# Performance work log

Measured on AMD Instinct MI355X. Metric: run time of the kernel, lower is better.

The kernel has to match this reference:

```python
import jax, jax.numpy as jnp
import numpy as np

BETA = 1.0
EPS_MU = 1e-6
EPS_LOG = 1e-8
D_DIM = 2048
M_EVENTS = 16384
T_HORIZON = 100


def setup_inputs() -> dict:
    key = jax.random.key(0)
    k1, k2 = jax.random.split(key)
    # sorted event times in [0, T_HORIZON)
    t_events = jnp.sort(jax.random.uniform(k1, (M_EVENTS,), jnp.float32) * T_HORIZON)
    marks = jax.random.randint(k2, (M_EVENTS,), 0, D_DIM)  # int marks in {0..D-1}
    # learned params, init exactly as in torch module
    log_mu = jnp.full((D_DIM,), -3.0, jnp.float32)
    log_alpha = jnp.full((D_DIM, D_DIM), -4.0, jnp.float32)
    return {
        "t_events": t_events,
        "marks": marks,
        "T_max": T_HORIZON,
        "log_mu": log_mu,
        "log_alpha": log_alpha,
    }


def _loglik(t_events, log_mu, log_alpha, marks, T_max, beta=BETA):
    mu = jax.nn.softplus(log_mu) + EPS_MU          # [D]
    alpha = jax.nn.softplus(log_alpha)             # [D, D]
    D = mu.shape[0]
    # dt[0] = 0 so the first step leaves S (= zeros) untouched, matching the
    # torch loop which skips decay at n == 0.
    dt = jnp.concatenate([jnp.zeros((1,), t_events.dtype), jnp.diff(t_events)])  # [M]

    def step(S, xs):
        dt_n, d = xs
        S = jnp.exp(-beta * dt_n) * S              # exponential decay of state [D]
        lam_d = mu[d] + alpha[d] @ S               # intensity at event's mark
        S = S.at[d].add(1.0)                       # self-excitation bump
        return S, jnp.log(lam_d + EPS_LOG)

    _, log_lams = jax.lax.scan(step, jnp.zeros((D,), mu.dtype), (dt, marks))

    # compensator integral term
    T = jnp.asarray(T_max, t_events.dtype)
    one_minus_exp = 1.0 - jnp.exp(-beta * (T - t_events))          # [M]
    contrib = jax.ops.segment_sum(one_minus_exp, marks, num_segments=D)  # [D]
    integral = mu * T + alpha @ (contrib / beta)                   # [D]
    return log_lams.sum() - integral.sum()


def reference(t_events, marks, T_max, log_mu, log_alpha):
    return _loglik(t_events, log_mu, log_alpha, marks, T_max)
```

## Files before the change

kernel.cpp:

```cpp
#include <hip/hip_runtime.h>
#include <math.h>

#define D_DIM 2048
#define M_EV  16384
#define LCH   32
#define CCH   (M_EV / LCH)
#define SEG   32
#define NSEG  (CCH / SEG)
#define BETA  1.0f

__device__ __forceinline__ float softplus_f(float x){
  float e = __expf(-fabsf(x));
  return fmaxf(x, 0.0f) + __logf(1.0f + e);
}

__device__ __forceinline__ unsigned short f2bf(float f){
  unsigned b = __float_as_uint(f);
  return (unsigned short)((b + 0x7FFFu + ((b >> 16) & 1u)) >> 16);
}
__device__ __forceinline__ float bf2f(unsigned short u){
  return __uint_as_float(((unsigned)u) << 16);
}

__device__ __forceinline__ float decode_T(const void* p){
  unsigned bits = *(const unsigned*)p;
  float fv = __uint_as_float(bits);
  return (fv >= 1e-3f && fv <= 1e7f) ? fv : (float)(int)bits;
}

__device__ __forceinline__ float wave_red(float v){
  #pragma unroll
  for (int o = 32; o > 0; o >>= 1) v += __shfl_down(v, o);
  return v;
}

__global__ void k_small(const float* __restrict__ t, const int* __restrict__ m,
                        const void* Tp, const float* __restrict__ log_mu,
                        float* __restrict__ muw, float* __restrict__ contrib,
                        float* __restrict__ SL, float* __restrict__ dchunk,
                        float* __restrict__ cumdec, float* __restrict__ Aseg,
                        float* __restrict__ acc){
  const int b = blockIdx.x, tid = threadIdx.x;
  if (b < 8){
    int j = b*256 + tid;
    float v = softplus_f(log_mu[j]) + 1e-6f;
    muw[j] = v;
    float s = wave_red(v);
    if ((tid & 63) == 0) atomicAdd(&acc[2], s);
  } else if (b < 72){
    int i = (b-8)*256 + tid;
    int d = m[i];
    float ti = t[i];
    float T = decode_T(Tp);
    atomicAdd(&contrib[d], 1.0f - __expf(-BETA * (T - ti)));
    int c = i >> 5;
    if (c < CCH - 1){
      float tn = t[(c+1)*LCH];
      atomicAdd(&SL[(size_t)c * D_DIM + d], __expf(-BETA * (tn - ti)));
    }
  } else {
    int c = (b-72)*256 + tid;
    float tc = t[c*LCH];
    dchunk[c] = (c < CCH-1) ? __expf(-BETA * (t[(c+1)*LCH] - tc)) : 1.0f;
    int s0c = (c >> 5) << 5;
    cumdec[c] = __expf(-BETA * (tc - t[s0c*LCH]));
    if (b == 72 && tid < NSEG){
      int s = tid;
      Aseg[s] = (s < NSEG-1)
        ? __expf(-BETA * (t[(s+1)*SEG*LCH] - t[s*SEG*LCH])) : 1.0f;
    }
  }
}

__global__ void k_scan_alpha(float* __restrict__ SL,
                             const float* __restrict__ dchunk,
                             float* __restrict__ Carry,
                             const float* __restrict__ la,
                             const float* __restrict__ contrib,
                             unsigned short* __restrict__ sA,
                             float* __restrict__ acc){
  const int b = blockIdx.x, tid = threadIdx.x;
  if (b < 128){
    const int seg = b >> 3, jb = b & 7;
    const int j = jb*256 + tid;
    const int c0 = seg * SEG;
    const size_t base = (size_t)c0 * D_DIM + j;
    float u = 0.f;
    float cur[4], nxt[4];
    #pragma unroll
    for (int q = 0; q < 4; ++q) cur[q] = SL[base + (size_t)q * D_DIM];
    for (int g = 0; g < SEG; g += 4){
      #pragma unroll
      for (int q = 0; q < 4; ++q)
        nxt[q] = (g+4 < SEG) ? SL[base + (size_t)(g+4+q) * D_DIM] : 0.f;
      #pragma unroll
      for (int q = 0; q < 4; ++q){
        int c = c0 + g + q;
        float l = cur[q];
        SL[(size_t)c * D_DIM + j] = u;
        u = fmaf(dchunk[c], u, l);
      }
      #pragma unroll
      for (int q = 0; q < 4; ++q) cur[q] = nxt[q];
    }
    Carry[(size_t)seg * D_DIM + j] = u;
    return;
  }
  const int nthreads = 512*256;
  int atid = (b-128)*256 + tid;
  const float4* la4 = (const float4*)la;
  ushort4* sA4 = (ushort4*)sA;
  float p = 0.f;
  #pragma unroll
  for (int u = 0; u < 8; ++u){
    int i4 = atid + u * nthreads;
    float4 x = la4[i4];
    float4 sp;
    sp.x = softplus_f(x.x); sp.y = softplus_f(x.y);
    sp.z = softplus_f(x.z); sp.w = softplus_f(x.w);
    ushort4 h;
    h.x = f2bf(sp.x); h.y = f2bf(sp.y); h.z = f2bf(sp.z); h.w = f2bf(sp.w);
    sA4[i4] = h;
    int col = (i4 * 4) & (D_DIM - 1);
    p = fmaf(sp.x, contrib[col+0], p);
    p = fmaf(sp.y, contrib[col+1], p);
    p = fmaf(sp.z, contrib[col+2], p);
    p = fmaf(sp.w, contrib[col+3], p);
  }
  __shared__ float red[4];
  float w = wave_red(p);
  int lane = tid & 63, wid = tid >> 6;
  if (lane == 0) red[wid] = w;
  __syncthreads();
  if (tid == 0) atomicAdd(&acc[1], red[0]+red[1]+red[2]+red[3]);
}

__global__ __launch_bounds__(512) void k_events(
    const float* __restrict__ t, const int* __restrict__ m,
    const unsigned short* __restrict__ sA, const float* __restrict__ muw,
    const float* __restrict__ SL, const float* __restrict__ Carry,
    const float* __restrict__ Aseg,
    const float* __restrict__ cumdec, float* __restrict__ acc,
    const void* Tp, float* __restrict__ out){
  __shared__ float S0[D_DIM];
  __shared__ float tl[LCH];
  __shared__ int   ml[LCH];
  __shared__ float wred[8];
  const int tid = threadIdx.x;
  const int c = blockIdx.x;
  const int seg = c >> 5;
  const float cd = cumdec[c];

  {
    const float4 sv = *(const float4*)(SL + (size_t)c * D_DIM + tid*4);
    float4 e = {0.f, 0.f, 0.f, 0.f};
    float wgt = 1.f;
    for (int s = seg - 1; s >= 0; --s){
      const float4 cr = *(const float4*)(Carry + (size_t)s * D_DIM + tid*4);
      e.x = fmaf(cr.x, wgt, e.x); e.y = fmaf(cr.y, wgt, e.y);
      e.z = fmaf(cr.z, wgt, e.z); e.w = fmaf(cr.w, wgt, e.w);
      wgt *= Aseg[s];
    }
    float4 s;
    s.x = fmaf(e.x, cd, sv.x); s.y = fmaf(e.y, cd, sv.y);
    s.z = fmaf(e.z, cd, sv.z); s.w = fmaf(e.w, cd, sv.w);
    *(float4*)&S0[tid*4] = s;
  }
  if (tid < LCH){
    ml[tid] = m[c*LCH + tid];
    tl[tid] = t[c*LCH + tid];
  }
  __syncthreads();

  const int l = tid & 63, w = tid >> 6;
  const int l4 = l * 4;

  float4 s0[8];
  #pragma unroll
  for (int u = 0; u < 8; ++u) s0[u] = *(const float4*)&S0[u*256 + l4];

  const float t0 = tl[0];
  float lgw = 0.f;
  #pragma unroll
  for (int q = 0; q < 4; ++q){
    const int k = w*4 + q;
    const int d = ml[k];
    const unsigned short* row = sA + (size_t)d * D_DIM;
    float p = 0.f;
    #pragma unroll
    for (int u = 0; u < 8; ++u){
      ushort4 a = *(const ushort4*)(row + u*256 + l4);
      p = fmaf(bf2f(a.x), s0[u].x, p);
      p = fmaf(bf2f(a.y), s0[u].y, p);
      p = fmaf(bf2f(a.z), s0[u].z, p);
      p = fmaf(bf2f(a.w), s0[u].w, p);
    }
    const float tk = tl[k];
    float g = 0.f;
    if (l < k) g = bf2f(row[ml[l]]) * __expf(tl[l] - tk);
    p = fmaf(p, __expf(t0 - tk), g);
    float v = wave_red(p);
    if (l == 0) lgw += __logf(muw[d] + v + 1e-8f);
  }
  if (l == 0) wred[w] = lgw;
  __syncthreads();
  if (tid == 0){
    float lg = ((wred[0]+wred[1])+(wred[2]+wred[3]))
             + ((wred[4]+wred[5])+(wred[6]+wred[7]));
    atomicAdd(&acc[0], lg);
    __threadfence();
    unsigned old = atomicAdd((unsigned*)&acc[3], 1u);
    if (old == CCH - 1){
      float a0 = atomicAdd(&acc[0], 0.0f);
      float a1 = atomicAdd(&acc[1], 0.0f);
      float a2 = atomicAdd(&acc[2], 0.0f);
      float T = decode_T(Tp);
      out[0] = a0 - (T * a2 + a1 * (1.0f / BETA));
    }
  }
}

extern "C" void kernel_launch(void* const* d_in, const int* in_sizes, int n_in,
                              void* d_out, int out_size, void* d_ws, size_t ws_size,
                              hipStream_t stream) {
  const float* t_events  = (const float*)d_in[0];
  const int*   marks     = (const int*)  d_in[1];
  const void*  Tp        =               d_in[2];
  const float* log_mu    = (const float*)d_in[3];
  const float* log_alpha = (const float*)d_in[4];
  float* out = (float*)d_out;

  float* ws      = (float*)d_ws;
  float* SL      = ws;
  float* contrib = SL + (size_t)CCH * D_DIM;
  float* acc     = contrib + D_DIM;
  float* Carry   = acc + 16;
  float* muw     = Carry + (size_t)NSEG * D_DIM;
  float* dchunk  = muw + D_DIM;
  float* cumdec  = dchunk + CCH;
  float* Aseg    = cumdec + CCH;
  unsigned short* sA = (unsigned short*)(Aseg + NSEG);

  size_t zero_floats = (size_t)CCH * D_DIM + D_DIM + 16;
  hipMemsetAsync(d_ws, 0, zero_floats * sizeof(float), stream);

  k_small     <<<74, 256, 0, stream>>>(t_events, marks, Tp, log_mu, muw,
                                       contrib, SL, dchunk, cumdec, Aseg, acc);
  k_scan_alpha<<<640, 256, 0, stream>>>(SL, dchunk, Carry, log_alpha,
                                        contrib, sA, acc);
  k_events    <<<CCH, 512, 0, stream>>>(t_events, marks, sA, muw,
                                        SL, Carry, Aseg, cumdec, acc, Tp, out);
}
```

Baseline: 113.5 us.

## Fuse memset and three kernels into one cooperative kernel with grid syncs

Replaces the memset plus three separate launches with a single cooperative kernel of 512 blocks × 256 threads. Grid-wide syncs separate the zeroing, prep, alpha-softplus/scan and event phases, and the final combine moves behind a last grid sync instead of an atomic counter. The aim is to remove launch gaps and the memset. In exchange it pays for several grid barriers, halves threads per block in the event phase (8 events per wave), and needs all 512 blocks to be co-resident.

```diff
diff --git a/kernel.cpp b/kernel.cpp
--- a/kernel.cpp
+++ b/kernel.cpp
@@ -1,4 +1,5 @@
 #include <hip/hip_runtime.h>
+#include <hip/hip_cooperative_groups.h>
 #include <math.h>
 
 #define D_DIM 2048
@@ -9,6 +10,12 @@
 #define NSEG  (CCH / SEG)
 #define BETA  1.0f
 
+#define NBLK  CCH
+#define NTHR  256
+#define TOTTHR (NBLK * NTHR)
+
+namespace cg = cooperative_groups;
+
 __device__ __forceinline__ float softplus_f(float x){
   float e = __expf(-fabsf(x));
   return fmaxf(x, 0.0f) + __logf(1.0f + e);
@@ -34,21 +41,38 @@
   return v;
 }
 
-__global__ void k_small(const float* __restrict__ t, const int* __restrict__ m,
-                        const void* Tp, const float* __restrict__ log_mu,
-                        float* __restrict__ muw, float* __restrict__ contrib,
-                        float* __restrict__ SL, float* __restrict__ dchunk,
-                        float* __restrict__ cumdec, float* __restrict__ Aseg,
-                        float* __restrict__ acc){
-  const int b = blockIdx.x, tid = threadIdx.x;
-  if (b < 8){
-    int j = b*256 + tid;
-    float v = softplus_f(log_mu[j]) + 1e-6f;
-    muw[j] = v;
+__global__ __launch_bounds__(NTHR, 2) void k_fused(
+    const float* __restrict__ t, const int* __restrict__ m,
+    const void* Tp, const float* __restrict__ log_mu,
+    const float* __restrict__ la,
+    float* __restrict__ muw, float* __restrict__ contrib,
+    float* __restrict__ SL, float* __restrict__ dchunk,
+    float* __restrict__ cumdec, float* __restrict__ Aseg,
+    float* __restrict__ Carry, unsigned short* __restrict__ sA,
+    float* __restrict__ acc, float* __restrict__ out)
+{
+  cg::grid_group grid = cg::this_grid();
+  const int b   = blockIdx.x;
+  const int tid = threadIdx.x;
+  const int gtid = b * NTHR + tid;
+
+  {
+    const float4 z = make_float4(0.f, 0.f, 0.f, 0.f);
+    float4* SL4 = (float4*)SL;
+    SL4[gtid] = z;
+    SL4[gtid + TOTTHR] = z;
+    if (gtid < D_DIM / 4) ((float4*)contrib)[gtid] = z;
+    if (gtid < 16) acc[gtid] = 0.f;
+  }
+  grid.sync();
+
+  if (gtid < 2048){
+    float v = softplus_f(log_mu[gtid]) + 1e-6f;
+    muw[gtid] = v;
     float s = wave_red(v);
     if ((tid & 63) == 0) atomicAdd(&acc[2], s);
-  } else if (b < 72){
-    int i = (b-8)*256 + tid;
+  } else if (gtid < 2048 + M_EV){
+    int i = gtid - 2048;
     int d = m[i];
     float ti = t[i];
     float T = decode_T(Tp);
@@ -58,34 +82,53 @@
       float tn = t[(c+1)*LCH];
       atomicAdd(&SL[(size_t)c * D_DIM + d], __expf(-BETA * (tn - ti)));
     }
-  } else {
-    int c = (b-72)*256 + tid;
+  } else if (gtid < 2048 + M_EV + CCH){
+    int c = gtid - (2048 + M_EV);
     float tc = t[c*LCH];
     dchunk[c] = (c < CCH-1) ? __expf(-BETA * (t[(c+1)*LCH] - tc)) : 1.0f;
     int s0c = (c >> 5) << 5;
     cumdec[c] = __expf(-BETA * (tc - t[s0c*LCH]));
-    if (b == 72 && tid < NSEG){
-      int s = tid;
-      Aseg[s] = (s < NSEG-1)
-        ? __expf(-BETA * (t[(s+1)*SEG*LCH] - t[s*SEG*LCH])) : 1.0f;
-    }
-  }
-}
-
-__global__ void k_scan_alpha(float* __restrict__ SL,
-                             const float* __restrict__ dchunk,
-                             float* __restrict__ Carry,
-                             const float* __restrict__ la,
-                             const float* __restrict__ contrib,
-                             unsigned short* __restrict__ sA,
-                             float* __restrict__ acc){
-  const int b = blockIdx.x, tid = threadIdx.x;
-  if (b < 128){
-    const int seg = b >> 3, jb = b & 7;
-    const int j = jb*256 + tid;
-    const int c0 = seg * SEG;
+  } else if (gtid < 2048 + M_EV + CCH + NSEG){
+    int s = gtid - (2048 + M_EV + CCH);
+    Aseg[s] = (s < NSEG-1)
+      ? __expf(-BETA * (t[(s+1)*SEG*LCH] - t[s*SEG*LCH])) : 1.0f;
+  }
+  grid.sync();
+
+  {
+    const float4* la4 = (const float4*)la;
+    ushort4* sA4 = (ushort4*)sA;
+    float p = 0.f;
+    #pragma unroll
+    for (int u = 0; u < 8; ++u){
+      int i4 = gtid + u * TOTTHR;
+      float4 x = la4[i4];
+      float4 sp;
+      sp.x = softplus_f(x.x); sp.y = softplus_f(x.y);
+      sp.z = softplus_f(x.z); sp.w = softplus_f(x.w);
+      ushort4 h;
+      h.x = f2bf(sp.x); h.y = f2bf(sp.y); h.z = f2bf(sp.z); h.w = f2bf(sp.w);
+      sA4[i4] = h;
+      int col = (i4 * 4) & (D_DIM - 1);
+      p = fmaf(sp.x, contrib[col+0], p);
+      p = fmaf(sp.y, contrib[col+1], p);
+      p = fmaf(sp.z, contrib[col+2], p);
+      p = fmaf(sp.w, contrib[col+3], p);
+    }
+    __shared__ float red[4];
+    float wsum = wave_red(p);
+    int lane = tid & 63, wid = tid >> 6;
+    if (lane == 0) red[wid] = wsum;
+    __syncthreads();
+    if (tid == 0) atomicAdd(&acc[1], red[0]+red[1]+red[2]+red[3]);
+  }
+
+  if (gtid < NSEG * D_DIM){
+    const int seg = gtid >> 11;
+    const int j   = gtid & (D_DIM - 1);
+    const int c0  = seg * SEG;
     const size_t base = (size_t)c0 * D_DIM + j;
-    float u = 0.f;
+    float u2 = 0.f;
     float cur[4], nxt[4];
     #pragma unroll
     for (int q = 0; q < 4; ++q) cur[q] = SL[base + (size_t)q * D_DIM];
@@ -97,126 +140,99 @@
       for (int q = 0; q < 4; ++q){
         int c = c0 + g + q;
         float l = cur[q];
-        SL[(size_t)c * D_DIM + j] = u;
-        u = fmaf(dchunk[c], u, l);
+        SL[(size_t)c * D_DIM + j] = u2;
+        u2 = fmaf(dchunk[c], u2, l);
       }
       #pragma unroll
       for (int q = 0; q < 4; ++q) cur[q] = nxt[q];
     }
-    Carry[(size_t)seg * D_DIM + j] = u;
-    return;
-  }
-  const int nthreads = 512*256;
-  int atid = (b-128)*256 + tid;
-  const float4* la4 = (const float4*)la;
-  ushort4* sA4 = (ushort4*)sA;
-  float p = 0.f;
-  #pragma unroll
-  for (int u = 0; u < 8; ++u){
-    int i4 = atid + u * nthreads;
-    float4 x = la4[i4];
-    float4 sp;
-    sp.x = softplus_f(x.x); sp.y = softplus_f(x.y);
-    sp.z = softplus_f(x.z); sp.w = softplus_f(x.w);
-    ushort4 h;
-    h.x = f2bf(sp.x); h.y = f2bf(sp.y); h.z = f2bf(sp.z); h.w = f2bf(sp.w);
-    sA4[i4] = h;
-    int col = (i4 * 4) & (D_DIM - 1);
-    p = fmaf(sp.x, contrib[col+0], p);
-    p = fmaf(sp.y, contrib[col+1], p);
-    p = fmaf(sp.z, contrib[col+2], p);
-    p = fmaf(sp.w, contrib[col+3], p);
-  }
-  __shared__ float red[4];
-  float w = wave_red(p);
-  int lane = tid & 63, wid = tid >> 6;
-  if (lane == 0) red[wid] = w;
-  __syncthreads();
-  if (tid == 0) atomicAdd(&acc[1], red[0]+red[1]+red[2]+red[3]);
-}
-
-__global__ __launch_bounds__(512) void k_events(
-    const float* __restrict__ t, const int* __restrict__ m,
-    const unsigned short* __restrict__ sA, const float* __restrict__ muw,
-    const float* __restrict__ SL, const float* __restrict__ Carry,
-    const float* __restrict__ Aseg,
-    const float* __restrict__ cumdec, float* __restrict__ acc,
-    const void* Tp, float* __restrict__ out){
-  __shared__ float S0[D_DIM];
-  __shared__ float tl[LCH];
-  __shared__ int   ml[LCH];
-  __shared__ float wred[8];
-  const int tid = threadIdx.x;
-  const int c = blockIdx.x;
-  const int seg = c >> 5;
-  const float cd = cumdec[c];
+    Carry[(size_t)seg * D_DIM + j] = u2;
+  }
+  grid.sync();
 
   {
-    const float4 sv = *(const float4*)(SL + (size_t)c * D_DIM + tid*4);
-    float4 e = {0.f, 0.f, 0.f, 0.f};
-    float wgt = 1.f;
-    for (int s = seg - 1; s >= 0; --s){
-      const float4 cr = *(const float4*)(Carry + (size_t)s * D_DIM + tid*4);
-      e.x = fmaf(cr.x, wgt, e.x); e.y = fmaf(cr.y, wgt, e.y);
-      e.z = fmaf(cr.z, wgt, e.z); e.w = fmaf(cr.w, wgt, e.w);
-      wgt *= Aseg[s];
-    }
-    float4 s;
-    s.x = fmaf(e.x, cd, sv.x); s.y = fmaf(e.y, cd, sv.y);
-    s.z = fmaf(e.z, cd, sv.z); s.w = fmaf(e.w, cd, sv.w);
-    *(float4*)&S0[tid*4] = s;
-  }
-  if (tid < LCH){
-    ml[tid] = m[c*LCH + tid];
-    tl[tid] = t[c*LCH + tid];
-  }
-  __syncthreads();
-
-  const int l = tid & 63, w = tid >> 6;
-  const int l4 = l * 4;
-
-  float4 s0[8];
-  #pragma unroll
-  for (int u = 0; u < 8; ++u) s0[u] = *(const float4*)&S0[u*256 + l4];
-
-  const float t0 = tl[0];
-  float lgw = 0.f;
-  #pragma unroll
-  for (int q = 0; q < 4; ++q){
-    const int k = w*4 + q;
-    const int d = ml[k];
-    const unsigned short* row = sA + (size_t)d * D_DIM;
-    float p = 0.f;
-    #pragma unroll
-    for (int u = 0; u < 8; ++u){
-      ushort4 a = *(const ushort4*)(row + u*256 + l4);
-      p = fmaf(bf2f(a.x), s0[u].x, p);
-      p = fmaf(bf2f(a.y), s0[u].y, p);
-      p = fmaf(bf2f(a.z), s0[u].z, p);
-      p = fmaf(bf2f(a.w), s0[u].w, p);
-    }
-    const float tk = tl[k];
-    float g = 0.f;
-    if (l < k) g = bf2f(row[ml[l]]) * __expf(tl[l] - tk);
-    p = fmaf(p, __expf(t0 - tk), g);
-    float v = wave_red(p);
-    if (l == 0) lgw += __logf(muw[d] + v + 1e-8f);
-  }
-  if (l == 0) wred[w] = lgw;
-  __syncthreads();
-  if (tid == 0){
-    float lg = ((wred[0]+wred[1])+(wred[2]+wred[3]))
-             + ((wred[4]+wred[5])+(wred[6]+wred[7]));
-    atomicAdd(&acc[0], lg);
-    __threadfence();
-    unsigned old = atomicAdd((unsigned*)&acc[3], 1u);
-    if (old == CCH - 1){
-      float a0 = atomicAdd(&acc[0], 0.0f);
-      float a1 = atomicAdd(&acc[1], 0.0f);
-      float a2 = atomicAdd(&acc[2], 0.0f);
-      float T = decode_T(Tp);
-      out[0] = a0 - (T * a2 + a1 * (1.0f / BETA));
-    }
+    __shared__ float S0[D_DIM];
+    __shared__ float tl[LCH];
+    __shared__ int   ml[LCH];
+    __shared__ float wred[4];
+    const int c = b;
+    const int seg = c >> 5;
+    const float cd = cumdec[c];
+    {
+      const size_t rowc = (size_t)c * D_DIM;
+      const int col = tid * 4;
+      float4 sv0 = *(const float4*)(SL + rowc + col);
+      float4 sv1 = *(const float4*)(SL + rowc + 1024 + col);
+      float4 e0 = make_float4(0,0,0,0), e1 = make_float4(0,0,0,0);
+      float wgt = 1.f;
+      for (int s = seg - 1; s >= 0; --s){
+        const float4 cr0 = *(const float4*)(Carry + (size_t)s * D_DIM + col);
+        const float4 cr1 = *(const float4*)(Carry + (size_t)s * D_DIM + 1024 + col);
+        e0.x = fmaf(cr0.x, wgt, e0.x); e0.y = fmaf(cr0.y, wgt, e0.y);
+        e0.z = fmaf(cr0.z, wgt, e0.z); e0.w = fmaf(cr0.w, wgt, e0.w);
+        e1.x = fmaf(cr1.x, wgt, e1.x); e1.y = fmaf(cr1.y, wgt, e1.y);
+        e1.z = fmaf(cr1.z, wgt, e1.z); e1.w = fmaf(cr1.w, wgt, e1.w);
+        wgt *= Aseg[s];
+      }
+      float4 o0, o1;
+      o0.x = fmaf(e0.x, cd, sv0.x); o0.y = fmaf(e0.y, cd, sv0.y);
+      o0.z = fmaf(e0.z, cd, sv0.z); o0.w = fmaf(e0.w, cd, sv0.w);
+      o1.x = fmaf(e1.x, cd, sv1.x); o1.y = fmaf(e1.y, cd, sv1.y);
+      o1.z = fmaf(e1.z, cd, sv1.z); o1.w = fmaf(e1.w, cd, sv1.w);
+      *(float4*)&S0[col]        = o0;
+      *(float4*)&S0[1024 + col] = o1;
+    }
+    if (tid < LCH){
+      ml[tid] = m[c*LCH + tid];
+      tl[tid] = t[c*LCH + tid];
+    }
+    __syncthreads();
+
+    const int l = tid & 63, w = tid >> 6;
+    const int l4 = l * 4;
+
+    float4 s0[8];
+    #pragma unroll
+    for (int u = 0; u < 8; ++u) s0[u] = *(const float4*)&S0[u*256 + l4];
+
+    const float t0 = tl[0];
+    float lgw = 0.f;
+    #pragma unroll
+    for (int q = 0; q < 8; ++q){
+      const int k = w*8 + q;
+      const int d = ml[k];
+      const unsigned short* row = sA + (size_t)d * D_DIM;
+      float p = 0.f;
+      #pragma unroll
+      for (int u = 0; u < 8; ++u){
+        ushort4 a = *(const ushort4*)(row + u*256 + l4);
+        p = fmaf(bf2f(a.x), s0[u].x, p);
+        p = fmaf(bf2f(a.y), s0[u].y, p);
+        p = fmaf(bf2f(a.z), s0[u].z, p);
+        p = fmaf(bf2f(a.w), s0[u].w, p);
+      }
+      const float tk = tl[k];
+      float g = 0.f;
+      if (l < k) g = bf2f(row[ml[l]]) * __expf(tl[l] - tk);
+      p = fmaf(p, __expf(t0 - tk), g);
+      float v = wave_red(p);
+      if (l == 0) lgw += __logf(muw[d] + v + 1e-8f);
+    }
+    if (l == 0) wred[w] = lgw;
+    __syncthreads();
+    if (tid == 0){
+      float lg = (wred[0]+wred[1]) + (wred[2]+wred[3]);
+      atomicAdd(&acc[0], lg);
+    }
+  }
+  grid.sync();
+
+  if (gtid == 0){
+    float a0 = atomicAdd(&acc[0], 0.0f);
+    float a1 = atomicAdd(&acc[1], 0.0f);
+    float a2 = atomicAdd(&acc[2], 0.0f);
+    float T = decode_T(Tp);
+    out[0] = a0 - (T * a2 + a1 * (1.0f / BETA));
   }
 }
 
@@ -241,13 +257,12 @@
   float* Aseg    = cumdec + CCH;
   unsigned short* sA = (unsigned short*)(Aseg + NSEG);
 
-  size_t zero_floats = (size_t)CCH * D_DIM + D_DIM + 16;
-  hipMemsetAsync(d_ws, 0, zero_floats * sizeof(float), stream);
-
-  k_small     <<<74, 256, 0, stream>>>(t_events, marks, Tp, log_mu, muw,
-                                       contrib, SL, dchunk, cumdec, Aseg, acc);
-  k_scan_alpha<<<640, 256, 0, stream>>>(SL, dchunk, Carry, log_alpha,
-                                        contrib, sA, acc);
-  k_events    <<<CCH, 512, 0, stream>>>(t_events, marks, sA, muw,
-                                        SL, Carry, Aseg, cumdec, acc, Tp, out);
-}
+  void* args[] = {
+    (void*)&t_events, (void*)&marks, (void*)&Tp, (void*)&log_mu,
+    (void*)&log_alpha, (void*)&muw, (void*)&contrib, (void*)&SL,
+    (void*)&dchunk, (void*)&cumdec, (void*)&Aseg, (void*)&Carry,
+    (void*)&sA, (void*)&acc, (void*)&out
+  };
+  hipLaunchCooperativeKernel((const void*)k_fused, dim3(NBLK), dim3(NTHR),
+                             args, 0, stream);
+}
```

Measured after the change: 330.7 us. 191% more time.

## Drop workspace memset by building chunk sums in LDS and reordering compensator

Applied to the files above, without the earlier changes.

Removes the large hipMemsetAsync over the SL buffer (CCH*D floats, about 4 MB). Each prep block now accumulates its 8 chunk rows in shared memory and writes them out whole. The compensator term changes from alpha@contrib to per-event column sums of alpha, which are accumulated into 8 sharded colsum arrays. The per-event dot against those sums is done in k_events, so the contrib scatter atomics go away. The cost is a 64KB LDS allocation in k_prep and extra colsum reads and atomics in the events kernel.

```diff
diff --git a/kernel.cpp b/kernel.cpp
--- a/kernel.cpp
+++ b/kernel.cpp
@@ -8,6 +8,7 @@
 #define SEG   32
 #define NSEG  (CCH / SEG)
 #define BETA  1.0f
+#define NSH   8
 
 __device__ __forceinline__ float softplus_f(float x){
   float e = __expf(-fabsf(x));
@@ -34,51 +35,65 @@
   return v;
 }
 
-__global__ void k_small(const float* __restrict__ t, const int* __restrict__ m,
-                        const void* Tp, const float* __restrict__ log_mu,
-                        float* __restrict__ muw, float* __restrict__ contrib,
-                        float* __restrict__ SL, float* __restrict__ dchunk,
-                        float* __restrict__ cumdec, float* __restrict__ Aseg,
-                        float* __restrict__ acc){
+__global__ __launch_bounds__(256) void k_prep(
+    const float* __restrict__ t, const int* __restrict__ m,
+    const float* __restrict__ log_mu,
+    float* __restrict__ muw, float* __restrict__ SL,
+    float* __restrict__ dchunk, float* __restrict__ cumdec,
+    float* __restrict__ Aseg, float* __restrict__ colsum,
+    float* __restrict__ acc)
+{
+  __shared__ float Srow[8 * D_DIM];
   const int b = blockIdx.x, tid = threadIdx.x;
   if (b < 8){
     int j = b*256 + tid;
     float v = softplus_f(log_mu[j]) + 1e-6f;
     muw[j] = v;
     float s = wave_red(v);
-    if ((tid & 63) == 0) atomicAdd(&acc[2], s);
+    if ((tid & 63) == 0) Srow[tid >> 6] = s;
+    __syncthreads();
+    if (tid == 0) acc[8 + b] = (Srow[0]+Srow[1]) + (Srow[2]+Srow[3]);
   } else if (b < 72){
-    int i = (b-8)*256 + tid;
-    int d = m[i];
-    float ti = t[i];
-    float T = decode_T(Tp);
-    atomicAdd(&contrib[d], 1.0f - __expf(-BETA * (T - ti)));
-    int c = i >> 5;
+    float4* S4 = (float4*)Srow;
+    const float4 z = make_float4(0.f,0.f,0.f,0.f);
+    #pragma unroll
+    for (int k = 0; k < 16; ++k) S4[k*256 + tid] = z;
+    __syncthreads();
+    const int i = (b-8)*256 + tid;
+    const int c = i >> 5;
     if (c < CCH - 1){
       float tn = t[(c+1)*LCH];
-      atomicAdd(&SL[(size_t)c * D_DIM + d], __expf(-BETA * (tn - ti)));
-    }
+      atomicAdd(&Srow[(tid >> 5)*D_DIM + m[i]], __expf(-BETA * (tn - t[i])));
+    }
+    __syncthreads();
+    float4* G4 = (float4*)(SL + (size_t)(b-8) * (8*D_DIM));
+    #pragma unroll
+    for (int k = 0; k < 16; ++k) G4[k*256 + tid] = S4[k*256 + tid];
   } else {
     int c = (b-72)*256 + tid;
     float tc = t[c*LCH];
     dchunk[c] = (c < CCH-1) ? __expf(-BETA * (t[(c+1)*LCH] - tc)) : 1.0f;
     int s0c = (c >> 5) << 5;
     cumdec[c] = __expf(-BETA * (tc - t[s0c*LCH]));
+    float4* C4 = (float4*)colsum;
+    const float4 z = make_float4(0.f,0.f,0.f,0.f);
+    int q0 = ((b-72)*256 + tid) * 8;
+    #pragma unroll
+    for (int k = 0; k < 8; ++k) C4[q0 + k] = z;
     if (b == 72 && tid < NSEG){
       int s = tid;
       Aseg[s] = (s < NSEG-1)
         ? __expf(-BETA * (t[(s+1)*SEG*LCH] - t[s*SEG*LCH])) : 1.0f;
     }
-  }
-}
-
-__global__ void k_scan_alpha(float* __restrict__ SL,
-                             const float* __restrict__ dchunk,
-                             float* __restrict__ Carry,
-                             const float* __restrict__ la,
-                             const float* __restrict__ contrib,
-                             unsigned short* __restrict__ sA,
-                             float* __restrict__ acc){
+    if (b == 73 && tid < 4) acc[tid] = 0.f;
+  }
+}
+
+__global__ __launch_bounds__(256) void k_scan_alpha(
+    float* __restrict__ SL, const float* __restrict__ dchunk,
+    float* __restrict__ Carry, const float* __restrict__ la,
+    unsigned short* __restrict__ sA, float* __restrict__ colsum)
+{
   const int b = blockIdx.x, tid = threadIdx.x;
   if (b < 128){
     const int seg = b >> 3, jb = b & 7;
@@ -110,7 +125,7 @@
   int atid = (b-128)*256 + tid;
   const float4* la4 = (const float4*)la;
   ushort4* sA4 = (ushort4*)sA;
-  float p = 0.f;
+  float p0=0.f, p1=0.f, p2=0.f, p3=0.f;
   #pragma unroll
   for (int u = 0; u < 8; ++u){
     int i4 = atid + u * nthreads;
@@ -121,26 +136,22 @@
     ushort4 h;
     h.x = f2bf(sp.x); h.y = f2bf(sp.y); h.z = f2bf(sp.z); h.w = f2bf(sp.w);
     sA4[i4] = h;
-    int col = (i4 * 4) & (D_DIM - 1);
-    p = fmaf(sp.x, contrib[col+0], p);
-    p = fmaf(sp.y, contrib[col+1], p);
-    p = fmaf(sp.z, contrib[col+2], p);
-    p = fmaf(sp.w, contrib[col+3], p);
-  }
-  __shared__ float red[4];
-  float w = wave_red(p);
-  int lane = tid & 63, wid = tid >> 6;
-  if (lane == 0) red[wid] = w;
-  __syncthreads();
-  if (tid == 0) atomicAdd(&acc[1], red[0]+red[1]+red[2]+red[3]);
+    p0 += sp.x; p1 += sp.y; p2 += sp.z; p3 += sp.w;
+  }
+  const int col = (atid * 4) & (D_DIM - 1);
+  float* cs = colsum + (size_t)(b & 7) * D_DIM;
+  atomicAdd(&cs[col+0], p0);
+  atomicAdd(&cs[col+1], p1);
+  atomicAdd(&cs[col+2], p2);
+  atomicAdd(&cs[col+3], p3);
 }
 
 __global__ __launch_bounds__(512) void k_events(
     const float* __restrict__ t, const int* __restrict__ m,
     const unsigned short* __restrict__ sA, const float* __restrict__ muw,
     const float* __restrict__ SL, const float* __restrict__ Carry,
-    const float* __restrict__ Aseg,
-    const float* __restrict__ cumdec, float* __restrict__ acc,
+    const float* __restrict__ Aseg, const float* __restrict__ cumdec,
+    const float* __restrict__ colsum, float* __restrict__ acc,
     const void* Tp, float* __restrict__ out){
   __shared__ float S0[D_DIM];
   __shared__ float tl[LCH];
@@ -171,6 +182,20 @@
     tl[tid] = t[c*LCH + tid];
   }
   __syncthreads();
+
+  if (tid < 64){
+    float v = 0.f;
+    if (tid < 32){
+      int d = ml[tid];
+      float cstot = 0.f;
+      #pragma unroll
+      for (int s = 0; s < NSH; ++s) cstot += colsum[s*D_DIM + d];
+      float T = decode_T(Tp);
+      v = cstot * (1.0f - __expf(-BETA * (T - tl[tid])));
+    }
+    v = wave_red(v);
+    if (tid == 0) atomicAdd(&acc[1], v);
+  }
 
   const int l = tid & 63, w = tid >> 6;
   const int l4 = l * 4;
@@ -213,9 +238,11 @@
     if (old == CCH - 1){
       float a0 = atomicAdd(&acc[0], 0.0f);
       float a1 = atomicAdd(&acc[1], 0.0f);
-      float a2 = atomicAdd(&acc[2], 0.0f);
+      float musum = 0.f;
+      #pragma unroll
+      for (int j = 8; j < 16; ++j) musum += atomicAdd(&acc[j], 0.0f);
       float T = decode_T(Tp);
-      out[0] = a0 - (T * a2 + a1 * (1.0f / BETA));
+      out[0] = a0 - (T * musum + a1 * (1.0f / BETA));
     }
   }
 }
@@ -232,22 +259,18 @@
 
   float* ws      = (float*)d_ws;
   float* SL      = ws;
-  float* contrib = SL + (size_t)CCH * D_DIM;
-  float* acc     = contrib + D_DIM;
-  float* Carry   = acc + 16;
+  float* Carry   = SL + (size_t)CCH * D_DIM;
   float* muw     = Carry + (size_t)NSEG * D_DIM;
   float* dchunk  = muw + D_DIM;
   float* cumdec  = dchunk + CCH;
   float* Aseg    = cumdec + CCH;
-  unsigned short* sA = (unsigned short*)(Aseg + NSEG);
-
-  size_t zero_floats = (size_t)CCH * D_DIM + D_DIM + 16;
-  hipMemsetAsync(d_ws, 0, zero_floats * sizeof(float), stream);
-
-  k_small     <<<74, 256, 0, stream>>>(t_events, marks, Tp, log_mu, muw,
-                                       contrib, SL, dchunk, cumdec, Aseg, acc);
-  k_scan_alpha<<<640, 256, 0, stream>>>(SL, dchunk, Carry, log_alpha,
-                                        contrib, sA, acc);
-  k_events    <<<CCH, 512, 0, stream>>>(t_events, marks, sA, muw,
-                                        SL, Carry, Aseg, cumdec, acc, Tp, out);
-}
+  float* colsum  = Aseg + NSEG;
+  float* acc     = colsum + (size_t)NSH * D_DIM;
+  unsigned short* sA = (unsigned short*)(acc + 16);
+
+  k_prep      <<<74, 256, 0, stream>>>(t_events, marks, log_mu, muw, SL,
+                                       dchunk, cumdec, Aseg, colsum, acc);
+  k_scan_alpha<<<640, 256, 0, stream>>>(SL, dchunk, Carry, log_alpha, sA, colsum);
+  k_events    <<<CCH, 512, 0, stream>>>(t_events, marks, sA, muw, SL, Carry,
+                                        Aseg, cumdec, colsum, acc, Tp, out);
+}
```

Result: slower. 131.8 us (+16.1%).
